# Optimization experiments

Measured on AMD Instinct MI355X. Metric: run time of the kernel, lower is better.

Reference implementation:

```python
import jax, jax.numpy as jnp
import numpy as np

B, C, H, W = 8, 64, 64, 64
CQ = C // 2

def setup_inputs() -> dict:
    key = jax.random.key(0)
    ks = jax.random.split(key, 10)
    s = 0.05
    return {
        "x": jax.random.normal(ks[0], (B, C, H, W), jnp.float32),
        "wq": jax.random.normal(ks[1], (CQ, C), jnp.float32) * s,
        "bq": jax.random.normal(ks[2], (CQ,), jnp.float32) * s,
        "wk": jax.random.normal(ks[3], (CQ, C), jnp.float32) * s,
        "bk": jax.random.normal(ks[4], (CQ,), jnp.float32) * s,
        "wv": jax.random.normal(ks[5], (C, C), jnp.float32) * s,
        "bv": jax.random.normal(ks[6], (C,), jnp.float32) * s,
        "wf": jax.random.normal(ks[7], (C, C), jnp.float32) * s,
        "bf": jax.random.normal(ks[8], (C,), jnp.float32) * s,
        "gamma": jnp.ones((1,), jnp.float32),
    }

def _conv1x1(w, b, x):
    # 1x1 conv == channel matmul: [O,C] x [B,C,H,W] -> [B,O,H,W]
    return jnp.einsum('oc,bchw->bohw', w, x) + b[None, :, None, None]

def reference(x, wq, bq, wk, bk, wv, bv, wf, bf, gamma):
    b, c, h, w = x.shape
    n = h * w
    q = _conv1x1(wq, bq, x).reshape(b, -1, n)   # [B, C/2, N]
    k = _conv1x1(wk, bk, x).reshape(b, -1, n)   # [B, C/2, N]
    v = _conv1x1(wv, bv, x).reshape(b, c, n)    # [B, C,   N]
    scale = 1.0 / jnp.sqrt(jnp.float32(n))
    energy = jnp.einsum('bcn,bcm->bnm', q, k) * scale  # [B, N, N]
    attn = jax.nn.softmax(energy, axis=-1)
    out = jnp.einsum('bcm,bnm->bcn', v, attn)          # V @ attn^T
    out = out.reshape(b, c, h, w)
    out = _conv1x1(wf, bf, out)
    return gamma[0] * out + x
```

## Files before the change

kernel.cpp:

```cpp
#include <hip/hip_runtime.h>

typedef unsigned short u16;
typedef unsigned int   u32;
typedef __bf16  bf16x8 __attribute__((ext_vector_type(8)));
typedef float   f32x16 __attribute__((ext_vector_type(16)));
typedef u32     u32x4  __attribute__((ext_vector_type(4)));

#define NN  4096
#define CCH 64
#define CQ  32
#define K1S 0.0225421092623961f

__device__ __forceinline__ u16 bfc(float a) { return __builtin_bit_cast(u16, (__bf16)a); }

__device__ __forceinline__ u32 e2pk(float a, float b) {
  float ea, eb; u32 r;
  asm("v_exp_f32 %0, %1" : "=v"(ea) : "v"(a));
  asm("v_exp_f32 %0, %1" : "=v"(eb) : "v"(b));
  asm("v_cvt_pk_bf16_f32 %0, %1, %2" : "=v"(r) : "v"(ea), "v"(eb));
  return r;
}

__device__ __forceinline__ void gload16(const void* g, void* l) {
  __builtin_amdgcn_global_load_lds((const __attribute__((address_space(1))) void*)g,
                                   (__attribute__((address_space(3))) void*)l, 16, 0, 0);
}


__global__ __launch_bounds__(512) void qkv_kernel(
    const float* __restrict__ x,
    const float* __restrict__ wq, const float* __restrict__ bq,
    const float* __restrict__ wk, const float* __restrict__ bk,
    const float* __restrict__ wv, const float* __restrict__ bv,
    u16* __restrict__ qT, char* __restrict__ kws, char* __restrict__ vws)
{
  __shared__ float xs[64][64];
  __shared__ u16 qls[64][34];
  __shared__ u16 kls[64][34];
  __shared__ u16 vls[64][66];
  const int bid = blockIdx.x;
  const int b = bid >> 6;
  const int chunk = bid & 63;
  const int nbase = chunk * 64;
  const int t = threadIdx.x, lane = t & 63, wid = t >> 6;

  {
    const float* xb = x + (size_t)b * CCH * NN + nbase;
    const int row = t >> 3, colq = (t & 7) * 2;
    float4 v0 = *(const float4*)(xb + (size_t)row * NN + colq * 4);
    float4 v1 = *(const float4*)(xb + (size_t)row * NN + colq * 4 + 4);
    float4* dst = (float4*)&xs[0][0];
    dst[row * 16 + colq]     = v0;
    dst[row * 16 + colq + 1] = v1;
  }
  __syncthreads();

  float xcol[64];
  #pragma unroll
  for (int c = 0; c < 64; ++c) xcol[c] = xs[c][lane];

  const float* w; const float* bias; float sc = 1.0f;
  const int sub = (wid & 1) * 16;
  if (wid < 2)      { w = wq + sub * 64; bias = bq + sub; sc = K1S; }
  else if (wid < 4) { w = wk + sub * 64; bias = bk + sub; }
  else              { w = wv + (wid - 4) * 16 * 64; bias = bv + (wid - 4) * 16; }

  #pragma unroll 2
  for (int i = 0; i < 16; ++i) {
    float a = bias[i];
    #pragma unroll
    for (int c = 0; c < 64; ++c) a = fmaf(w[i * 64 + c], xcol[c], a);
    a *= sc;
    u16 hv = bfc(a);
    if (wid < 2)      qls[lane][sub + i] = hv;
    else if (wid < 4) kls[lane][sub + i] = hv;
    else              vls[(wid - 4) * 16 + i][lane] = hv;
  }
  __syncthreads();

  u32* qdst = (u32*)(qT + ((size_t)b * NN + nbase) * CQ);
  #pragma unroll
  for (int jj = 0; jj < 2; ++jj) {
    int i = t + 512 * jj;
    int n = i >> 4, cp = i & 15;
    qdst[i] = *(const u32*)&qls[n][cp * 2];
  }
  u32* kimg = (u32*)(kws + ((size_t)b * 64 + chunk) * 4096);
  #pragma unroll
  for (int jj = 0; jj < 2; ++jj) {
    int i = t + 512 * jj;
    int reg = i >> 8, l = (i >> 2) & 63, j2 = i & 3;
    int s = reg >> 1, ks = reg & 1;
    int key = s * 32 + (l & 31);
    int ck  = ks * 16 + (l >> 5) * 8 + j2 * 2;
    kimg[i] = *(const u32*)&kls[key][ck];
  }
  u32* vimg = (u32*)(vws + ((size_t)b * 64 + chunk) * 8192);
  #pragma unroll
  for (int jj = 0; jj < 4; ++jj) {
    int i = t + 512 * jj;
    int reg = i >> 8, l = (i >> 2) & 63, j2 = i & 3;
    int s = reg >> 2, kb = (reg >> 1) & 1, ct = reg & 1;
    int c   = ct * 32 + (l & 31);
    int key = s * 32 + kb * 16 + (l >> 5) * 4 + (j2 >> 1) * 8 + (j2 & 1) * 2;
    vimg[i] = *(const u32*)&vls[c][key];
  }
}

template<int NSPLIT>
__global__ __launch_bounds__(256, 2) void attn_kernel(
    const u16* __restrict__ qT, const char* __restrict__ kws, const char* __restrict__ vws,
    u32* __restrict__ opart, float* __restrict__ lpart)
{
  constexpr int CH = 64 / NSPLIT;
  constexpr int MH = CH / 2;
  __shared__ __align__(16) char kbuf[3][8192];
  __shared__ __align__(16) char vbuf[3][16384];
  const int bid = blockIdx.x;
  const int b = bid & 7, qt = (bid >> 3) & 15, split = bid >> 7;
  const int t = threadIdx.x, lane = t & 63, wid = t >> 6;
  const int h = lane >> 5, c31 = lane & 31;

  const u16* qpA = qT + ((size_t)b * NN + qt * 256 + wid * 64 + c31) * CQ + h * 8;
  const bf16x8 qfA0 = *(const bf16x8*)(qpA);
  const bf16x8 qfA1 = *(const bf16x8*)(qpA + 16);
  const bf16x8 qfB0 = *(const bf16x8*)(qpA + 32 * CQ);
  const bf16x8 qfB1 = *(const bf16x8*)(qpA + 32 * CQ + 16);

  const char* ksrc = kws + ((size_t)b * 64 + split * CH) * 4096 + t * 16;
  const char* vsrc = vws + ((size_t)b * 64 + split * CH) * 8192 + t * 16;

  auto stage = [&](int buf, int m) {
    const char* kc = ksrc + (size_t)m * 8192;
    const char* vc = vsrc + (size_t)m * 16384;
    gload16(kc,         &kbuf[buf][wid * 1024]);
    gload16(kc + 4096,  &kbuf[buf][4096 + wid * 1024]);
    gload16(vc,         &vbuf[buf][wid * 1024]);
    gload16(vc + 4096,  &vbuf[buf][4096 + wid * 1024]);
    gload16(vc + 8192,  &vbuf[buf][8192 + wid * 1024]);
    gload16(vc + 12288, &vbuf[buf][12288 + wid * 1024]);
  };

  const bf16x8 onef = __builtin_bit_cast(bf16x8,
      (u32x4){0x3F803F80u, 0x3F803F80u, 0x3F803F80u, 0x3F803F80u});

  f32x16 accA0 = {}, accA1 = {}, accB0 = {}, accB1 = {}, laccA = {}, laccB = {};
  const int lofs = lane * 16;

  stage(0, 0);
  stage(1, 1);

  #pragma unroll
  for (int m = 0; m < MH; ++m) {
    if (m == MH - 1) asm volatile("s_waitcnt vmcnt(0)" ::: "memory");
    else             asm volatile("s_waitcnt vmcnt(6)" ::: "memory");
    __builtin_amdgcn_s_barrier();
    __builtin_amdgcn_sched_barrier(0);
    if (m + 2 < MH) stage((m + 2) % 3, m + 2);
    const int cur = m % 3;

    #pragma unroll
    for (int sub = 0; sub < 2; ++sub) {
      const char* kb = &kbuf[cur][sub * 4096];
      const char* vb = &vbuf[cur][sub * 8192];

      const bf16x8 kf0 = *(const bf16x8*)&kb[lofs];
      const bf16x8 kf1 = *(const bf16x8*)&kb[1024 + lofs];
      const bf16x8 kf2 = *(const bf16x8*)&kb[2048 + lofs];
      const bf16x8 kf3 = *(const bf16x8*)&kb[3072 + lofs];

      f32x16 sA0, sA1, sB0, sB1;
      __builtin_amdgcn_s_setprio(1);
      sA0 = __builtin_amdgcn_mfma_f32_32x32x16_bf16(kf0, qfA0, (f32x16){}, 0, 0, 0);
      sA0 = __builtin_amdgcn_mfma_f32_32x32x16_bf16(kf1, qfA1, sA0, 0, 0, 0);
      sA1 = __builtin_amdgcn_mfma_f32_32x32x16_bf16(kf2, qfA0, (f32x16){}, 0, 0, 0);
      sA1 = __builtin_amdgcn_mfma_f32_32x32x16_bf16(kf3, qfA1, sA1, 0, 0, 0);
      sB0 = __builtin_amdgcn_mfma_f32_32x32x16_bf16(kf0, qfB0, (f32x16){}, 0, 0, 0);
      sB0 = __builtin_amdgcn_mfma_f32_32x32x16_bf16(kf1, qfB1, sB0, 0, 0, 0);
      sB1 = __builtin_amdgcn_mfma_f32_32x32x16_bf16(kf2, qfB0, (f32x16){}, 0, 0, 0);
      sB1 = __builtin_amdgcn_mfma_f32_32x32x16_bf16(kf3, qfB1, sB1, 0, 0, 0);
      __builtin_amdgcn_s_setprio(0);

      u32 pwA[16] __attribute__((aligned(16)));
      u32 pwB[16] __attribute__((aligned(16)));
      #pragma unroll
      for (int r = 0; r < 16; r += 2) {
        pwA[r >> 1]       = e2pk(sA0[r], sA0[r + 1]);
        pwA[8 + (r >> 1)] = e2pk(sA1[r], sA1[r + 1]);
        pwB[r >> 1]       = e2pk(sB0[r], sB0[r + 1]);
        pwB[8 + (r >> 1)] = e2pk(sB1[r], sB1[r + 1]);
      }

      __builtin_amdgcn_s_setprio(1);
      #pragma unroll
      for (int s = 0; s < 2; ++s) {
        #pragma unroll
        for (int kb2 = 0; kb2 < 2; ++kb2) {
          const bf16x8 pfA = __builtin_bit_cast(bf16x8, *(const u32x4*)&pwA[s * 8 + kb2 * 4]);
          const bf16x8 pfB = __builtin_bit_cast(bf16x8, *(const u32x4*)&pwB[s * 8 + kb2 * 4]);
          const bf16x8 vf0 = *(const bf16x8*)&vb[(s * 4 + kb2 * 2) * 1024 + lofs];
          const bf16x8 vf1 = *(const bf16x8*)&vb[(s * 4 + kb2 * 2 + 1) * 1024 + lofs];
          accA0 = __builtin_amdgcn_mfma_f32_32x32x16_bf16(vf0, pfA, accA0, 0, 0, 0);
          accA1 = __builtin_amdgcn_mfma_f32_32x32x16_bf16(vf1, pfA, accA1, 0, 0, 0);
          accB0 = __builtin_amdgcn_mfma_f32_32x32x16_bf16(vf0, pfB, accB0, 0, 0, 0);
          accB1 = __builtin_amdgcn_mfma_f32_32x32x16_bf16(vf1, pfB, accB1, 0, 0, 0);
          laccA = __builtin_amdgcn_mfma_f32_32x32x16_bf16(onef, pfA, laccA, 0, 0, 0);
          laccB = __builtin_amdgcn_mfma_f32_32x32x16_bf16(onef, pfB, laccB, 0, 0, 0);
        }
      }
      __builtin_amdgcn_s_setprio(0);
    }
  }

  const int qt128 = qt * 2 + (wid >> 1);
  const size_t obase = ((size_t)(b * 32 + qt128) * NSPLIT + split) * 4096;
  #pragma unroll
  for (int j = 0; j < 2; ++j) {
    const int col = (wid & 1) * 64 + j * 32 + c31;
    #pragma unroll
    for (int ct = 0; ct < 2; ++ct) {
      const f32x16& a = j ? (ct ? accB1 : accB0) : (ct ? accA1 : accA0);
      #pragma unroll
      for (int g2 = 0; g2 < 4; ++g2) {
        #pragma unroll
        for (int b2 = 0; b2 < 2; ++b2) {
          int cp = ct * 16 + g2 * 4 + h * 2 + b2;
          float lo = a[g2 * 4 + b2 * 2], hi = a[g2 * 4 + b2 * 2 + 1];
          u32 pr; asm("v_cvt_pk_bf16_f32 %0, %1, %2" : "=v"(pr) : "v"(lo), "v"(hi));
          opart[obase + cp * 128 + col] = pr;
        }
      }
    }
    if (h == 0) {
      const f32x16& l = j ? laccB : laccA;
      lpart[((size_t)(b * 32 + qt128) * NSPLIT + split) * 128 + col] = l[0];
    }
  }
}

template<int NSPLIT>
__global__ __launch_bounds__(512) void combine_kernel(
    const u32* __restrict__ opart, const float* __restrict__ lpart,
    const float* __restrict__ x, const float* __restrict__ wf, const float* __restrict__ bfb,
    const float* __restrict__ gamma, float* __restrict__ out)
{
  __shared__ float ols[64][65];
  __shared__ float linv[64];
  const int bid = blockIdx.x;
  const int b = bid & 7, qt64 = bid >> 3;
  const int qt128 = qt64 >> 1, qh = qt64 & 1;
  const int t = threadIdx.x, lane = t & 63, wid = t >> 6;

  const u32* ob = opart + (size_t)(b * 32 + qt128) * NSPLIT * 4096 + qh * 64;
  #pragma unroll
  for (int jj = 0; jj < 4; ++jj) {
    int i = t + 512 * jj;
    int cp = i >> 6, q = i & 63;
    float lo = 0.f, hi = 0.f;
    #pragma unroll
    for (int s = 0; s < NSPLIT; ++s) {
      u32 a = ob[s * 4096 + cp * 128 + q];
      lo += __builtin_bit_cast(float, (a << 16));
      hi += __builtin_bit_cast(float, (a & 0xffff0000u));
    }
    ols[cp * 2][q]     = lo;
    ols[cp * 2 + 1][q] = hi;
  }
  if (t < 64) {
    const float* lp = lpart + (size_t)(b * 32 + qt128) * NSPLIT * 128 + qh * 64;
    float l = 0.f;
    #pragma unroll
    for (int s = 0; s < NSPLIT; ++s) l += lp[s * 128 + t];
    linv[t] = 1.f / l;
  }
  __syncthreads();

  const float oinv = linv[lane];
  float oc[64];
  #pragma unroll
  for (int c = 0; c < 64; ++c) oc[c] = ols[c][lane] * oinv;
  const float gm = gamma[0];
  const size_t nidx = (size_t)qt64 * 64 + lane;
  #pragma unroll
  for (int i = 0; i < 8; ++i) {
    const int o = wid * 8 + i;
    float a = bfb[o];
    #pragma unroll
    for (int c = 0; c < 64; ++c) a = fmaf(wf[o * 64 + c], oc[c], a);
    const size_t idx = ((size_t)b * CCH + o) * NN + nidx;
    out[idx] = gm * a + x[idx];
  }
}

extern "C" void kernel_launch(void* const* d_in, const int* in_sizes, int n_in,
                              void* d_out, int out_size, void* d_ws, size_t ws_size,
                              hipStream_t stream) {
  const float* x     = (const float*)d_in[0];
  const float* wq    = (const float*)d_in[1];
  const float* bq    = (const float*)d_in[2];
  const float* wk    = (const float*)d_in[3];
  const float* bk    = (const float*)d_in[4];
  const float* wv    = (const float*)d_in[5];
  const float* bv    = (const float*)d_in[6];
  const float* wf    = (const float*)d_in[7];
  const float* bf_   = (const float*)d_in[8];
  const float* gamma = (const float*)d_in[9];
  float* out = (float*)d_out;

  u16* qT   = (u16*)d_ws;
  char* kws = (char*)(qT + (size_t)8 * NN * CQ);
  char* vws = kws + (size_t)8 * 64 * 4096;
  u32* opart = (u32*)(vws + (size_t)8 * 64 * 8192);
  const size_t base = 2097152ull + 2097152ull + 4194304ull;
  const size_t need4 = base + 4ull * (4194304ull + 131072ull);

  qkv_kernel<<<dim3(512), dim3(512), 0, stream>>>(x, wq, bq, wk, bk, wv, bv, qT, kws, vws);
  if (ws_size >= need4) {
    float* lpart = (float*)(opart + (size_t)8 * 32 * 4 * 4096);
    attn_kernel<4><<<dim3(512), dim3(256), 0, stream>>>(qT, kws, vws, opart, lpart);
    combine_kernel<4><<<dim3(512), dim3(512), 0, stream>>>(opart, lpart, x, wf, bf_, gamma, out);
  } else {
    float* lpart = (float*)(opart + (size_t)8 * 32 * 2 * 4096);
    attn_kernel<2><<<dim3(256), dim3(256), 0, stream>>>(qT, kws, vws, opart, lpart);
    combine_kernel<2><<<dim3(512), dim3(512), 0, stream>>>(opart, lpart, x, wf, bf_, gamma, out);
  }
}
```

Before: 89.81 us.

## Compute softmax row sums with VALU adds, raise occupancy, add 8-way key split

Replaces the two ones-vector MFMAs per step that accumulated softmax denominators with scalar float adds of the fp32 exponentials, reduced across the lane halves by a shuffle at the end. It splits score computation into A and B halves to lower register pressure, raises launch bounds to 3 blocks per SM, and adds an NSPLIT=8 path with 1024 blocks when the workspace allows. The aim is fewer matrix-core instructions and more parallelism, at the cost of extra VALU work, more partial outputs for the combine kernel to read, and row sums taken from unrounded fp32 values rather than the bf16 values used in the PV product.

```diff
diff --git a/kernel.cpp b/kernel.cpp
--- a/kernel.cpp
+++ b/kernel.cpp
@@ -13,10 +13,11 @@
 
 __device__ __forceinline__ u16 bfc(float a) { return __builtin_bit_cast(u16, (__bf16)a); }
 
-__device__ __forceinline__ u32 e2pk(float a, float b) {
+__device__ __forceinline__ u32 e2pk_s(float a, float b, float& ps) {
   float ea, eb; u32 r;
   asm("v_exp_f32 %0, %1" : "=v"(ea) : "v"(a));
   asm("v_exp_f32 %0, %1" : "=v"(eb) : "v"(b));
+  ps += ea + eb;
   asm("v_cvt_pk_bf16_f32 %0, %1, %2" : "=v"(r) : "v"(ea), "v"(eb));
   return r;
 }
@@ -108,7 +109,7 @@
 }
 
 template<int NSPLIT>
-__global__ __launch_bounds__(256, 2) void attn_kernel(
+__global__ __launch_bounds__(256, 3) void attn_kernel(
     const u16* __restrict__ qT, const char* __restrict__ kws, const char* __restrict__ vws,
     u32* __restrict__ opart, float* __restrict__ lpart)
 {
@@ -141,10 +142,8 @@
     gload16(vc + 12288, &vbuf[buf][12288 + wid * 1024]);
   };
 
-  const bf16x8 onef = __builtin_bit_cast(bf16x8,
-      (u32x4){0x3F803F80u, 0x3F803F80u, 0x3F803F80u, 0x3F803F80u});
-
-  f32x16 accA0 = {}, accA1 = {}, accB0 = {}, accB1 = {}, laccA = {}, laccB = {};
+  f32x16 accA0 = {}, accA1 = {}, accB0 = {}, accB1 = {};
+  float lsumA = 0.f, lsumB = 0.f;
   const int lofs = lane * 16;
 
   stage(0, 0);
@@ -169,26 +168,36 @@
       const bf16x8 kf2 = *(const bf16x8*)&kb[2048 + lofs];
       const bf16x8 kf3 = *(const bf16x8*)&kb[3072 + lofs];
 
-      f32x16 sA0, sA1, sB0, sB1;
-      __builtin_amdgcn_s_setprio(1);
-      sA0 = __builtin_amdgcn_mfma_f32_32x32x16_bf16(kf0, qfA0, (f32x16){}, 0, 0, 0);
-      sA0 = __builtin_amdgcn_mfma_f32_32x32x16_bf16(kf1, qfA1, sA0, 0, 0, 0);
-      sA1 = __builtin_amdgcn_mfma_f32_32x32x16_bf16(kf2, qfA0, (f32x16){}, 0, 0, 0);
-      sA1 = __builtin_amdgcn_mfma_f32_32x32x16_bf16(kf3, qfA1, sA1, 0, 0, 0);
-      sB0 = __builtin_amdgcn_mfma_f32_32x32x16_bf16(kf0, qfB0, (f32x16){}, 0, 0, 0);
-      sB0 = __builtin_amdgcn_mfma_f32_32x32x16_bf16(kf1, qfB1, sB0, 0, 0, 0);
-      sB1 = __builtin_amdgcn_mfma_f32_32x32x16_bf16(kf2, qfB0, (f32x16){}, 0, 0, 0);
-      sB1 = __builtin_amdgcn_mfma_f32_32x32x16_bf16(kf3, qfB1, sB1, 0, 0, 0);
-      __builtin_amdgcn_s_setprio(0);
-
       u32 pwA[16] __attribute__((aligned(16)));
       u32 pwB[16] __attribute__((aligned(16)));
-      #pragma unroll
-      for (int r = 0; r < 16; r += 2) {
-        pwA[r >> 1]       = e2pk(sA0[r], sA0[r + 1]);
-        pwA[8 + (r >> 1)] = e2pk(sA1[r], sA1[r + 1]);
-        pwB[r >> 1]       = e2pk(sB0[r], sB0[r + 1]);
-        pwB[8 + (r >> 1)] = e2pk(sB1[r], sB1[r + 1]);
+
+      {
+        f32x16 sA0, sA1;
+        __builtin_amdgcn_s_setprio(1);
+        sA0 = __builtin_amdgcn_mfma_f32_32x32x16_bf16(kf0, qfA0, (f32x16){}, 0, 0, 0);
+        sA0 = __builtin_amdgcn_mfma_f32_32x32x16_bf16(kf1, qfA1, sA0, 0, 0, 0);
+        sA1 = __builtin_amdgcn_mfma_f32_32x32x16_bf16(kf2, qfA0, (f32x16){}, 0, 0, 0);
+        sA1 = __builtin_amdgcn_mfma_f32_32x32x16_bf16(kf3, qfA1, sA1, 0, 0, 0);
+        __builtin_amdgcn_s_setprio(0);
+        #pragma unroll
+        for (int r = 0; r < 16; r += 2) {
+          pwA[r >> 1]       = e2pk_s(sA0[r], sA0[r + 1], lsumA);
+          pwA[8 + (r >> 1)] = e2pk_s(sA1[r], sA1[r + 1], lsumA);
+        }
+      }
+      {
+        f32x16 sB0, sB1;
+        __builtin_amdgcn_s_setprio(1);
+        sB0 = __builtin_amdgcn_mfma_f32_32x32x16_bf16(kf0, qfB0, (f32x16){}, 0, 0, 0);
+        sB0 = __builtin_amdgcn_mfma_f32_32x32x16_bf16(kf1, qfB1, sB0, 0, 0, 0);
+        sB1 = __builtin_amdgcn_mfma_f32_32x32x16_bf16(kf2, qfB0, (f32x16){}, 0, 0, 0);
+        sB1 = __builtin_amdgcn_mfma_f32_32x32x16_bf16(kf3, qfB1, sB1, 0, 0, 0);
+        __builtin_amdgcn_s_setprio(0);
+        #pragma unroll
+        for (int r = 0; r < 16; r += 2) {
+          pwB[r >> 1]       = e2pk_s(sB0[r], sB0[r + 1], lsumB);
+          pwB[8 + (r >> 1)] = e2pk_s(sB1[r], sB1[r + 1], lsumB);
+        }
       }
 
       __builtin_amdgcn_s_setprio(1);
@@ -204,13 +213,14 @@
           accA1 = __builtin_amdgcn_mfma_f32_32x32x16_bf16(vf1, pfA, accA1, 0, 0, 0);
           accB0 = __builtin_amdgcn_mfma_f32_32x32x16_bf16(vf0, pfB, accB0, 0, 0, 0);
           accB1 = __builtin_amdgcn_mfma_f32_32x32x16_bf16(vf1, pfB, accB1, 0, 0, 0);
-          laccA = __builtin_amdgcn_mfma_f32_32x32x16_bf16(onef, pfA, laccA, 0, 0, 0);
-          laccB = __builtin_amdgcn_mfma_f32_32x32x16_bf16(onef, pfB, laccB, 0, 0, 0);
         }
       }
       __builtin_amdgcn_s_setprio(0);
     }
   }
+
+  lsumA += __shfl_xor(lsumA, 32, 64);
+  lsumB += __shfl_xor(lsumB, 32, 64);
 
   const int qt128 = qt * 2 + (wid >> 1);
   const size_t obase = ((size_t)(b * 32 + qt128) * NSPLIT + split) * 4096;
@@ -231,10 +241,8 @@
         }
       }
     }
-    if (h == 0) {
-      const f32x16& l = j ? laccB : laccA;
-      lpart[((size_t)(b * 32 + qt128) * NSPLIT + split) * 128 + col] = l[0];
-    }
+    if (h == 0)
+      lpart[((size_t)(b * 32 + qt128) * NSPLIT + split) * 128 + col] = j ? lsumB : lsumA;
   }
 }
 
@@ -312,10 +320,15 @@
   char* vws = kws + (size_t)8 * 64 * 4096;
   u32* opart = (u32*)(vws + (size_t)8 * 64 * 8192);
   const size_t base = 2097152ull + 2097152ull + 4194304ull;
+  const size_t need8 = base + 8ull * (4194304ull + 131072ull);
   const size_t need4 = base + 4ull * (4194304ull + 131072ull);
 
   qkv_kernel<<<dim3(512), dim3(512), 0, stream>>>(x, wq, bq, wk, bk, wv, bv, qT, kws, vws);
-  if (ws_size >= need4) {
+  if (ws_size >= need8) {
+    float* lpart = (float*)(opart + (size_t)8 * 32 * 8 * 4096);
+    attn_kernel<8><<<dim3(1024), dim3(256), 0, stream>>>(qT, kws, vws, opart, lpart);
+    combine_kernel<8><<<dim3(512), dim3(512), 0, stream>>>(opart, lpart, x, wf, bf_, gamma, out);
+  } else if (ws_size >= need4) {
     float* lpart = (float*)(opart + (size_t)8 * 32 * 4 * 4096);
     attn_kernel<4><<<dim3(512), dim3(256), 0, stream>>>(qT, kws, vws, opart, lpart);
     combine_kernel<4><<<dim3(512), dim3(512), 0, stream>>>(opart, lpart, x, wf, bf_, gamma, out);
```

Measured after the change: 95.47 us. 6.3% more time.
